# Optimization experiments

Measured on AMD Instinct MI355X. Metric: run time of the kernel, lower is better.

The kernel has to match this reference:

```python
import jax, jax.numpy as jnp
import numpy as np

B, T, D = 32, 512, 512
MAX_DUR = 8               # durations drawn from [0, MAX_DUR)
MAX_FRAMES = T * (MAX_DUR - 1)  # 3584 -> static upper bound on expanded length; pad to it
MAX_FRAMES = 4096          # round up to a nice static size


def setup_inputs() -> dict:
    key = jax.random.key(0)
    kx, kd = jax.random.split(key)
    x = jax.random.normal(kx, (B, T, D), dtype=jnp.float32)
    durations = jax.random.randint(kd, (B, T), 0, MAX_DUR, dtype=jnp.int32)
    return {"x": x, "durations": durations}


def reference(x, durations):
    # x: [B, T, D] float, durations: [B, T] int
    # Expansion via cumsum offsets + searchsorted gather (fused equivalent of
    # the host loop of repeat/cat/pad in the torch module).
    ends = jnp.cumsum(durations, axis=1)          # [B, T] exclusive end offsets
    total = ends[:, -1]                            # [B] true expanded lengths
    pos = jnp.arange(MAX_FRAMES, dtype=ends.dtype) # [F]
    # frame p belongs to token t where starts[t] <= p < ends[t]
    idx = jax.vmap(lambda e: jnp.searchsorted(e, pos, side='right'))(ends)  # [B, F]
    idx = jnp.clip(idx, 0, x.shape[1] - 1)
    out = jnp.take_along_axis(x, idx[:, :, None], axis=1)  # [B, F, D]
    mask = pos[None, :] < total[:, None]                    # [B, F]
    out = out * mask[:, :, None].astype(out.dtype)          # zero-pad beyond mel_len
    # torch fallback: an all-zero-duration row yields one zero frame, len 1
    mel_lens = jnp.maximum(total, 1).astype(jnp.int32)
    return out, mel_lens
```

## Files before the change

### kernel.cpp

```cpp
#include <hip/hip_runtime.h>
#include <hip/hip_bf16.h>

#define B_ 32
#define T_ 512
#define D_ 512
#define MAXF_ 4096

__global__ __launch_bounds__(512) void lr_scan_idx_kernel(const int* __restrict__ dur,
                                                          int* __restrict__ idx_map,
                                                          float* __restrict__ mel_out) {
    __shared__ int s[T_];
    const int b = blockIdx.x;
    const int t = threadIdx.x;
    s[t] = dur[b * T_ + t];
    __syncthreads();
    #pragma unroll
    for (int off = 1; off < T_; off <<= 1) {
        int tmp = (t >= off) ? s[t - off] : 0;
        __syncthreads();
        s[t] += tmp;
        __syncthreads();
    }
    const int total = s[T_ - 1];
    if (t == T_ - 1) {
        mel_out[b] = (float)(total > 1 ? total : 1);
    }
    for (int p = t; p < MAXF_; p += T_) {
        int v = -1;
        if (p < total) {
            int lo = 0, hi = T_;
            while (lo < hi) {
                int mid = (lo + hi) >> 1;
                if (s[mid] <= p) lo = mid + 1;
                else hi = mid;
            }
            v = lo < (T_ - 1) ? lo : (T_ - 1);
        }
        idx_map[b * MAXF_ + p] = v;
    }
}

__global__ __launch_bounds__(256) void lr_gather_kernel(const float4* __restrict__ x,
                                                        const int* __restrict__ idx_map,
                                                        float4* __restrict__ out) {
    const size_t gid = (size_t)blockIdx.x * 256 + threadIdx.x;
    const int frame = (int)(gid >> 7);
    const int c = (int)(gid & 127);
    const int idx = idx_map[frame];
    float4 v;
    if (idx < 0) {
        v = make_float4(0.f, 0.f, 0.f, 0.f);
    } else {
        const int b = frame >> 12;
        v = x[((size_t)(b * T_ + idx) << 7) + c];
    }
    out[gid] = v;
}

extern "C" void kernel_launch(void* const* d_in, const int* in_sizes, int n_in,
                              void* d_out, int out_size, void* d_ws, size_t ws_size,
                              hipStream_t stream) {
    const float* x = (const float*)d_in[0];
    const int* durations = (const int*)d_in[1];
    float* out = (float*)d_out;
    float* mel_out = out + (size_t)B_ * MAXF_ * D_;
    int* idx_map = (int*)d_ws;

    lr_scan_idx_kernel<<<B_, T_, 0, stream>>>(durations, idx_map, mel_out);

    const size_t n_vec4 = (size_t)B_ * MAXF_ * (D_ / 4);
    lr_gather_kernel<<<(int)(n_vec4 / 256), 256, 0, stream>>>(
        (const float4*)x, idx_map, (float4*)out);
}
```

Before: 306.4 us.

## Scatter index map directly, unroll gather per thread, use nontemporal stores

The prep kernel drops the per-frame binary search. Each token thread now writes its own index into its frame range, and the threads fill the tail past the total with -1. The gather kernel has each thread handle 8 float4 elements, so the grid is 8x smaller, and writes the output with nontemporal stores to avoid polluting the cache with the 256MB output stream. The scatter writes are uncoalesced and vary in length per thread, but the prep kernel is small next to the gather.

```diff
diff --git a/kernel.cpp b/kernel.cpp
--- a/kernel.cpp
+++ b/kernel.cpp
@@ -6,13 +6,16 @@
 #define D_ 512
 #define MAXF_ 4096
 
-__global__ __launch_bounds__(512) void lr_scan_idx_kernel(const int* __restrict__ dur,
-                                                          int* __restrict__ idx_map,
-                                                          float* __restrict__ mel_out) {
+typedef float f4 __attribute__((ext_vector_type(4)));
+
+__global__ __launch_bounds__(512) void lr_prep_kernel(const int* __restrict__ dur,
+                                                      int* __restrict__ idx_map,
+                                                      float* __restrict__ mel_out) {
     __shared__ int s[T_];
     const int b = blockIdx.x;
     const int t = threadIdx.x;
-    s[t] = dur[b * T_ + t];
+    const int d = dur[b * T_ + t];
+    s[t] = d;
     __syncthreads();
     #pragma unroll
     for (int off = 1; off < T_; off <<= 1) {
@@ -21,40 +24,35 @@
         s[t] += tmp;
         __syncthreads();
     }
+    const int end = s[t];
+    const int start = end - d;
     const int total = s[T_ - 1];
     if (t == T_ - 1) {
         mel_out[b] = (float)(total > 1 ? total : 1);
     }
-    for (int p = t; p < MAXF_; p += T_) {
-        int v = -1;
-        if (p < total) {
-            int lo = 0, hi = T_;
-            while (lo < hi) {
-                int mid = (lo + hi) >> 1;
-                if (s[mid] <= p) lo = mid + 1;
-                else hi = mid;
-            }
-            v = lo < (T_ - 1) ? lo : (T_ - 1);
-        }
-        idx_map[b * MAXF_ + p] = v;
-    }
+    int* __restrict__ im = idx_map + b * MAXF_;
+    for (int p = start; p < end; ++p) im[p] = t;
+    for (int p = total + t; p < MAXF_; p += T_) im[p] = -1;
 }
 
-__global__ __launch_bounds__(256) void lr_gather_kernel(const float4* __restrict__ x,
+#define CHUNK_V4 2048
+__global__ __launch_bounds__(256) void lr_gather_kernel(const f4* __restrict__ x,
                                                         const int* __restrict__ idx_map,
-                                                        float4* __restrict__ out) {
-    const size_t gid = (size_t)blockIdx.x * 256 + threadIdx.x;
-    const int frame = (int)(gid >> 7);
-    const int c = (int)(gid & 127);
-    const int idx = idx_map[frame];
-    float4 v;
-    if (idx < 0) {
-        v = make_float4(0.f, 0.f, 0.f, 0.f);
-    } else {
-        const int b = frame >> 12;
-        v = x[((size_t)(b * T_ + idx) << 7) + c];
+                                                        f4* __restrict__ out) {
+    const size_t base = (size_t)blockIdx.x * CHUNK_V4 + threadIdx.x;
+    #pragma unroll
+    for (int k = 0; k < 8; ++k) {
+        const size_t g = base + (size_t)k * 256;
+        const int frame = (int)(g >> 7);
+        const int c = (int)(g & 127);
+        const int idx = idx_map[frame];
+        f4 v = {0.f, 0.f, 0.f, 0.f};
+        if (idx >= 0) {
+            const int b = frame >> 12;
+            v = x[((size_t)(b * T_ + idx) << 7) + c];
+        }
+        __builtin_nontemporal_store(v, &out[g]);
     }
-    out[gid] = v;
 }
 
 extern "C" void kernel_launch(void* const* d_in, const int* in_sizes, int n_in,
@@ -66,9 +64,9 @@
     float* mel_out = out + (size_t)B_ * MAXF_ * D_;
     int* idx_map = (int*)d_ws;
 
-    lr_scan_idx_kernel<<<B_, T_, 0, stream>>>(durations, idx_map, mel_out);
+    lr_prep_kernel<<<B_, T_, 0, stream>>>(durations, idx_map, mel_out);
 
     const size_t n_vec4 = (size_t)B_ * MAXF_ * (D_ / 4);
-    lr_gather_kernel<<<(int)(n_vec4 / 256), 256, 0, stream>>>(
-        (const float4*)x, idx_map, (float4*)out);
+    lr_gather_kernel<<<(int)(n_vec4 / CHUNK_V4), 256, 0, stream>>>(
+        (const f4*)x, idx_map, (f4*)out);
 }
```

Result: faster. 298.7 us (-2.5%).
